# Optimization experiments

Measured on AMD Instinct MI355X. Metric: run time of the kernel, lower is better.

Reference implementation:

```python
import jax, jax.numpy as jnp
import numpy as np

BATCH, SEQ = 256, 100
DM = 256           # d_m
DI = 512           # Mamba d_inner = 2*d_m
DID = 512          # decoder d_inner = 2*d_d
N = 16             # d_state
DTR = 16           # dt_rank = ceil(d_m/16)
DCONV = 4
NLAYERS = 3


def silu(v):
    return v * jax.nn.sigmoid(v)


def setup_inputs() -> dict:
    key = jax.random.key(0)
    ks = jax.random.split(key, 20)
    rn = lambda k, s, sc=0.02: jax.random.normal(k, s, jnp.float32) * sc
    A_log = jnp.log(jnp.arange(1, N + 1, dtype=jnp.float32))  # (N,)
    return {
        'x': jax.random.normal(ks[0], (BATCH, SEQ, 8), jnp.float32),
        'W_embed': rn(ks[1], (8, DM)), 'b_embed': jnp.zeros((DM,), jnp.float32),
        'm_in_w': rn(ks[2], (DM, 2 * DI)),
        'm_conv_w': rn(ks[3], (DI, DCONV), 0.1), 'm_conv_b': jnp.zeros((DI,), jnp.float32),
        'm_xproj_w': rn(ks[4], (DI, DTR + 2 * N)),
        'm_dtproj_w': rn(ks[5], (DTR, DI), DTR ** -0.5),
        'm_dtproj_b': rn(ks[6], (DI,), 0.5) - 4.0,
        'm_A_log': jnp.broadcast_to(A_log, (DI, N)).copy(),
        'm_D': jnp.ones((DI,), jnp.float32),
        'm_out_w': rn(ks[7], (DI, DM)),
        'dec_in_w': rn(ks[8], (NLAYERS, 4, 2 * DID)), 'dec_in_b': jnp.zeros((NLAYERS, 2 * DID), jnp.float32),
        'dec_flow_w': rn(ks[9], (NLAYERS, DM, DTR + 2 * N)),
        'dec_dt_w': rn(ks[10], (NLAYERS, DTR, DID), DTR ** -0.5),
        'dec_dt_b': rn(ks[11], (NLAYERS, DID), 0.5) - 4.0,
        'dec_A_log': jnp.broadcast_to(A_log, (NLAYERS, DID, N)).copy(),
        'dec_D': jnp.ones((NLAYERS, DID), jnp.float32),
        'dec_out_w': rn(ks[12], (NLAYERS, DID, 4)), 'dec_out_b': jnp.zeros((NLAYERS, 4), jnp.float32),
    }


def _forward(x, W_embed, b_embed, m_in_w, m_conv_w, m_conv_b, m_xproj_w,
             m_dtproj_w, m_dtproj_b, m_A_log, m_D, m_out_w,
             dec_in_w, dec_in_b, dec_flow_w, dec_dt_w, dec_dt_b,
             dec_A_log, dec_D, dec_out_w, dec_out_b):
    b, l, _ = x.shape
    # ---- MambaEncoder ----
    emb = x @ W_embed + b_embed                       # (b, l, dm)
    xz = emb @ m_in_w                                 # (b, l, 2*di)
    xs, z = jnp.split(xz, 2, axis=-1)
    # causal depthwise conv1d, kernel=DCONV
    xp = jnp.pad(xs, ((0, 0), (DCONV - 1, 0), (0, 0)))
    xc = sum(xp[:, k:k + l, :] * m_conv_w[:, k] for k in range(DCONV)) + m_conv_b
    xc = silu(xc)
    proj = xc @ m_xproj_w                             # (b, l, dtr+2n)
    dt = jax.nn.softplus(proj[..., :DTR] @ m_dtproj_w + m_dtproj_b)  # (b, l, di)
    Bm = proj[..., DTR:DTR + N]                       # (b, l, n)
    Cm = proj[..., DTR + N:]
    A = -jnp.exp(m_A_log)                             # (di, n)

    def enc_step(h, inp):
        dt_t, B_t, C_t, x_t = inp                     # (b,di),(b,n),(b,n),(b,di)
        h = h * jnp.exp(dt_t[:, :, None] * A) + (dt_t * x_t)[:, :, None] * B_t[:, None, :]
        y = jnp.einsum('bdn,bn->bd', h, C_t) + m_D * x_t
        return h, y

    h0 = jnp.zeros((b, DI, N), xc.dtype)
    _, ys = jax.lax.scan(enc_step, h0,
                         (dt.transpose(1, 0, 2), Bm.transpose(1, 0, 2),
                          Cm.transpose(1, 0, 2), xc.transpose(1, 0, 2)))
    y = ys.transpose(1, 0, 2) * silu(z)               # (b, l, di)
    enc = y @ m_out_w                                 # (b, l, dm)
    flow = enc[:, -1]                                 # (b, dm) -- last token (no cls_token)

    # ---- FlowDecoder stack ----
    cur_bbox = x[:, -1, :4]
    hidden = jnp.zeros((b, DID, N), x.dtype)

    def dec_step(carry, p):
        bbox, h = carry
        in_w, in_b, flow_w, dt_w, dt_b, A_log, Dp, out_w, out_b = p
        bh = bbox @ in_w + in_b                       # (b, 2*did)
        e, r = jnp.split(bh, 2, axis=-1)
        e = silu(e)
        pf = flow @ flow_w                            # (b, dtr+2n)
        dtd = jax.nn.softplus(pf[:, :DTR] @ dt_w + dt_b)  # (b, did)
        Bp, Cp = pf[:, DTR:DTR + N], pf[:, DTR + N:]
        Ad = -jnp.exp(A_log)                          # (did, n)
        h = h * jnp.exp(dtd[:, :, None] * Ad) + e[:, :, None] * (dtd[:, :, None] * Bp[:, None, :])
        yd = jnp.einsum('bdn,bn->bd', h, Cp) + Dp * e
        yd = yd * silu(r)
        out = yd @ out_w + out_b                      # (b, 4)
        # torch code detaches cur_bbox and hidden_state between layers
        return (jax.lax.stop_gradient(out), jax.lax.stop_gradient(h)), out

    _, outs = jax.lax.scan(dec_step, (cur_bbox, hidden),
                           (dec_in_w, dec_in_b, dec_flow_w, dec_dt_w, dec_dt_b,
                            dec_A_log, dec_D, dec_out_w, dec_out_b))
    return outs[-1]                                   # final predicted bbox (b, 4)


def reference(x, W_embed, b_embed, m_in_w, m_conv_w, m_conv_b, m_xproj_w,
              m_dtproj_w, m_dtproj_b, m_A_log, m_D, m_out_w,
              dec_in_w, dec_in_b, dec_flow_w, dec_dt_w, dec_dt_b,
              dec_A_log, dec_D, dec_out_w, dec_out_b):
    return _forward(x, W_embed, b_embed, m_in_w, m_conv_w, m_conv_b, m_xproj_w,
                    m_dtproj_w, m_dtproj_b, m_A_log, m_D, m_out_w,
                    dec_in_w, dec_in_b, dec_flow_w, dec_dt_w, dec_dt_b,
                    dec_A_log, dec_D, dec_out_w, dec_out_b)
```

## Files before the change

### kernel.cpp

```cpp
#include <hip/hip_runtime.h>
#include <math.h>

#define BATCH 256
#define SEQ 100
#define DMODEL 256
#define DI 512
#define DID 512
#define NST 16
#define DTRANK 16
#define DCONV 4
#define NLAYERS 3

#define W2_OFF 0
#define B2_OFF 8192
#define WT_OFF 9216
#define CWT_OFF 33792
#define FLAG_OFF 35840
#define PROJ_OFF 35848
#define SILUZ_OFF 1264648
#define Y_OFF 1395720

__device__ __forceinline__ float silu_f(float x) { return x / (1.0f + __expf(-x)); }

#define DPP_ADD(v, ctrl, rmask) \
    v += __int_as_float(__builtin_amdgcn_update_dpp(0, __float_as_int(v), ctrl, rmask, 0xF, false))

__device__ __forceinline__ float wave64_sum(float v) {
    DPP_ADD(v, 0xB1, 0xF);
    DPP_ADD(v, 0x4E, 0xF);
    DPP_ADD(v, 0x141, 0xF);
    DPP_ADD(v, 0x140, 0xF);
    DPP_ADD(v, 0x142, 0xA);
    DPP_ADD(v, 0x143, 0xC);
    return v;
}

typedef float sf16 __attribute__((ext_vector_type(16)));
typedef float sf8 __attribute__((ext_vector_type(8)));

__device__ __forceinline__ int rfl(int v) { return __builtin_amdgcn_readfirstlane(v); }

#define SL2(dA, dB, base, offA, offB)                    \
    asm volatile("s_load_dwordx16 %0, %2, %3\n\t"        \
                 "s_load_dwordx16 %1, %2, %4"            \
                 : "=&s"(dA), "=&s"(dB)                  \
                 : "s"(base), "s"(offA), "s"(offB))
#define SLX(dX, base, off) \
    asm volatile("s_load_dwordx8 %0, %1, %2" : "=&s"(dX) : "s"(base), "s"(off))
#define SLC(dC, base, off) \
    asm volatile("s_load_dwordx16 %0, %1, %2" : "=&s"(dC) : "s"(base), "s"(off))
#define SL_WAIT()                                          \
    do {                                                   \
        asm volatile("s_waitcnt lgkmcnt(0)" ::: "memory"); \
        __builtin_amdgcn_sched_barrier(0);                 \
    } while (0)

__global__ void k_prep(const float* __restrict__ W_embed, const float* __restrict__ b_embed,
                       const float* __restrict__ m_in_w, const float* __restrict__ xproj_w,
                       const float* __restrict__ conv_w, const float* __restrict__ A_log,
                       const float* __restrict__ dec_A_log, float* __restrict__ ws,
                       int* __restrict__ flags) {
    int bid = blockIdx.x, tid = threadIdx.x;
    if (bid < 4) {
        int j = bid * 256 + tid;
        float acc[8] = {0, 0, 0, 0, 0, 0, 0, 0};
        float accb = 0.f;
        for (int c = 0; c < DMODEL; ++c) {
            float w = m_in_w[c * 1024 + j];
            accb += b_embed[c] * w;
#pragma unroll
            for (int i = 0; i < 8; ++i) acc[i] += W_embed[i * DMODEL + c] * w;
        }
#pragma unroll
        for (int i = 0; i < 8; ++i) ws[W2_OFF + i * 1024 + j] = acc[i];
        ws[B2_OFF + j] = accb;
    } else if (bid < 100) {
        int idx = (bid - 4) * 256 + tid;
        int j = idx / 512, c = idx % 512;
        ws[WT_OFF + j * 512 + c] = xproj_w[c * 48 + j];
    } else if (bid < 108) {
        int idx = (bid - 100) * 256 + tid;
        int tap = idx / 512, c = idx % 512;
        ws[CWT_OFF + tap * 512 + c] = conv_w[c * 4 + tap];
    } else {
        __shared__ int oks[2];
        if (tid == 0) { oks[0] = 1; oks[1] = 1; }
        __syncthreads();
        int bad_e = 0, bad_d = 0;
        for (int i = tid; i < DI * NST; i += 256) {
            int dd = i / NST, n = i % NST;
            float a0 = __expf(A_log[dd * NST]);
            float an = __expf(A_log[dd * NST + n]);
            if (fabsf(an - (n + 1) * a0) > 1e-4f * (n + 1)) bad_e = 1;
        }
        for (int i = tid; i < NLAYERS * DID * NST; i += 256) {
            int dd = i / NST, n = i % NST;
            float a0 = __expf(dec_A_log[dd * NST]);
            float an = __expf(dec_A_log[dd * NST + n]);
            if (fabsf(an - (n + 1) * a0) > 1e-4f * (n + 1)) bad_d = 1;
        }
        if (bad_e) atomicAnd(&oks[0], 0);
        if (bad_d) atomicAnd(&oks[1], 0);
        __syncthreads();
        if (tid == 0) { flags[0] = oks[0]; flags[1] = oks[1]; }
    }
}

__global__ void __launch_bounds__(256, 3) k_convproj(
    const float* __restrict__ x, const float* __restrict__ ws, const float* __restrict__ conv_b,
    float* __restrict__ proj_g, float* __restrict__ silu_z) {
    __shared__ __align__(16) float xs_s[23 * 512];
    __shared__ __align__(16) float proj_s[20 * 48];
    const float* W2 = ws + W2_OFF;
    const float* b2 = ws + B2_OFF;
    const float* wT = ws + WT_OFF;
    const float* cwT = ws + CWT_OFF;
    const int b = blockIdx.x / 5, tb = blockIdx.x % 5, t0 = tb * 20;
    const int tid = threadIdx.x, lane = tid & 63, wv = tid >> 6;

    {
        int c0 = tid * 2;
        float wa[8], wb[8];
#pragma unroll
        for (int i = 0; i < 8; ++i) {
            float2 wp = *(const float2*)&W2[i * 1024 + c0];
            wa[i] = wp.x;
            wb[i] = wp.y;
        }
        float2 bp = *(const float2*)&b2[c0];
        for (int r = 0; r < 23; ++r) {
            int t = t0 - 3 + r;
            float va = 0.f, vb = 0.f;
            if (t >= 0) {
                const float4* xr = (const float4*)(x + (size_t)(b * SEQ + t) * 8);
                float4 xlo = xr[0], xhi = xr[1];
                va = bp.x + xlo.x * wa[0] + xlo.y * wa[1] + xlo.z * wa[2] + xlo.w * wa[3] +
                     xhi.x * wa[4] + xhi.y * wa[5] + xhi.z * wa[6] + xhi.w * wa[7];
                vb = bp.y + xlo.x * wb[0] + xlo.y * wb[1] + xlo.z * wb[2] + xlo.w * wb[3] +
                     xhi.x * wb[4] + xhi.y * wb[5] + xhi.z * wb[6] + xhi.w * wb[7];
            }
            *(float2*)&xs_s[r * 512 + c0] = make_float2(va, vb);
        }
        if (tb == 4) {
            const float4* xr = (const float4*)(x + (size_t)(b * SEQ + SEQ - 1) * 8);
            float4 xlo = xr[0], xhi = xr[1];
            float za = b2[512 + c0], zb = b2[512 + c0 + 1];
#pragma unroll
            for (int i = 0; i < 8; ++i) {
                float xi = (i < 4) ? ((const float*)&xlo)[i] : ((const float*)&xhi)[i - 4];
                float2 wp = *(const float2*)&W2[i * 1024 + 512 + c0];
                za += xi * wp.x;
                zb += xi * wp.y;
            }
            silu_z[b * DI + c0] = silu_f(za);
            silu_z[b * DI + c0 + 1] = silu_f(zb);
        }
    }
    __syncthreads();
    const int cA = lane * 4, cB = 256 + lane * 4;
    float xcv[5][8];
    {
        float4 cwA[4], cwB[4];
#pragma unroll
        for (int tap = 0; tap < 4; ++tap) {
            cwA[tap] = *(const float4*)&cwT[tap * 512 + cA];
            cwB[tap] = *(const float4*)&cwT[tap * 512 + cB];
        }
        float4 cbA = *(const float4*)&conv_b[cA];
        float4 cbB = *(const float4*)&conv_b[cB];
#pragma unroll
        for (int q = 0; q < 5; ++q) {
            int rb = wv * 5 + q;
            float4 aA = cbA, aB = cbB;
#pragma unroll
            for (int tap = 0; tap < 4; ++tap) {
                float4 xA = *(const float4*)&xs_s[(rb + tap) * 512 + cA];
                float4 xB = *(const float4*)&xs_s[(rb + tap) * 512 + cB];
                aA.x += cwA[tap].x * xA.x; aA.y += cwA[tap].y * xA.y;
                aA.z += cwA[tap].z * xA.z; aA.w += cwA[tap].w * xA.w;
                aB.x += cwB[tap].x * xB.x; aB.y += cwB[tap].y * xB.y;
                aB.z += cwB[tap].z * xB.z; aB.w += cwB[tap].w * xB.w;
            }
            xcv[q][0] = silu_f(aA.x); xcv[q][1] = silu_f(aA.y);
            xcv[q][2] = silu_f(aA.z); xcv[q][3] = silu_f(aA.w);
            xcv[q][4] = silu_f(aB.x); xcv[q][5] = silu_f(aB.y);
            xcv[q][6] = silu_f(aB.z); xcv[q][7] = silu_f(aB.w);
        }
    }
    {
#pragma unroll 2
        for (int j = 0; j < 48; ++j) {
            float4 wA = *(const float4*)&wT[j * 512 + cA];
            float4 wB = *(const float4*)&wT[j * 512 + cB];
            float a0 = 0.f, a1 = 0.f, a2 = 0.f, a3 = 0.f, a4 = 0.f;
#pragma unroll
            for (int k = 0; k < 4; ++k) {
                float wk = ((const float*)&wA)[k];
                float wk2 = ((const float*)&wB)[k];
                a0 += xcv[0][k] * wk + xcv[0][4 + k] * wk2;
                a1 += xcv[1][k] * wk + xcv[1][4 + k] * wk2;
                a2 += xcv[2][k] * wk + xcv[2][4 + k] * wk2;
                a3 += xcv[3][k] * wk + xcv[3][4 + k] * wk2;
                a4 += xcv[4][k] * wk + xcv[4][4 + k] * wk2;
            }
            a0 = wave64_sum(a0); a1 = wave64_sum(a1); a2 = wave64_sum(a2);
            a3 = wave64_sum(a3); a4 = wave64_sum(a4);
            if (lane == 63) {
                proj_s[(wv * 5 + 0) * 48 + j] = a0;
                proj_s[(wv * 5 + 1) * 48 + j] = a1;
                proj_s[(wv * 5 + 2) * 48 + j] = a2;
                proj_s[(wv * 5 + 3) * 48 + j] = a3;
                proj_s[(wv * 5 + 4) * 48 + j] = a4;
            }
        }
    }
    __syncthreads();
    if (tid < 240) {
        float4* dst = (float4*)(proj_g + (size_t)(b * SEQ + t0) * 48);
        dst[tid] = ((const float4*)proj_s)[tid];
    }
}

#define SCAN_STEP(SA, SB, SX)                                                        \
    do {                                                                             \
        float xsv = biasc;                                                           \
        xsv = fmaf((SX)[0], w2c[0], xsv); xsv = fmaf((SX)[1], w2c[1], xsv);          \
        xsv = fmaf((SX)[2], w2c[2], xsv); xsv = fmaf((SX)[3], w2c[3], xsv);          \
        xsv = fmaf((SX)[4], w2c[4], xsv); xsv = fmaf((SX)[5], w2c[5], xsv);          \
        xsv = fmaf((SX)[6], w2c[6], xsv); xsv = fmaf((SX)[7], w2c[7], xsv);          \
        float cv = cb + win0 * cw0 + win1 * cw1 + win2 * cw2 + xsv * cw3;            \
        win0 = win1; win1 = win2; win2 = xsv;                                        \
        xcv = silu_f(cv);                                                            \
        float acc = bdt;                                                             \
        acc = fmaf((SA)[0], wr[0], acc);  acc = fmaf((SA)[1], wr[1], acc);           \
        acc = fmaf((SA)[2], wr[2], acc);  acc = fmaf((SA)[3], wr[3], acc);           \
        acc = fmaf((SA)[4], wr[4], acc);  acc = fmaf((SA)[5], wr[5], acc);           \
        acc = fmaf((SA)[6], wr[6], acc);  acc = fmaf((SA)[7], wr[7], acc);           \
        acc = fmaf((SA)[8], wr[8], acc);  acc = fmaf((SA)[9], wr[9], acc);           \
        acc = fmaf((SA)[10], wr[10], acc); acc = fmaf((SA)[11], wr[11], acc);        \
        acc = fmaf((SA)[12], wr[12], acc); acc = fmaf((SA)[13], wr[13], acc);        \
        acc = fmaf((SA)[14], wr[14], acc); acc = fmaf((SA)[15], wr[15], acc);        \
        float dtv = (acc > 20.f) ? acc : __logf(1.f + __expf(acc));                  \
        S += dtv;                                                                    \
        float sv = dtv * xcv;                                                        \
        if (fast) {                                                                  \
            float E1 = __expf(dtv * An0);                                            \
            float E2 = E1 * E1, E3 = E2 * E1, E4 = E2 * E2;                          \
            float E5 = E4 * E1, E6 = E4 * E2, E7 = E4 * E3, E8 = E4 * E4;            \
            float E9 = E8 * E1, E10 = E8 * E2, E11 = E8 * E3, E12 = E8 * E4;         \
            float E13 = E8 * E5, E14 = E8 * E6, E15 = E8 * E7, E16 = E8 * E8;        \
            h[0] = fmaf(h[0], E1, sv * (SB)[0]);   h[1] = fmaf(h[1], E2, sv * (SB)[1]); \
            h[2] = fmaf(h[2], E3, sv * (SB)[2]);   h[3] = fmaf(h[3], E4, sv * (SB)[3]); \
            h[4] = fmaf(h[4], E5, sv * (SB)[4]);   h[5] = fmaf(h[5], E6, sv * (SB)[5]); \
            h[6] = fmaf(h[6], E7, sv * (SB)[6]);   h[7] = fmaf(h[7], E8, sv * (SB)[7]); \
            h[8] = fmaf(h[8], E9, sv * (SB)[8]);   h[9] = fmaf(h[9], E10, sv * (SB)[9]); \
            h[10] = fmaf(h[10], E11, sv * (SB)[10]); h[11] = fmaf(h[11], E12, sv * (SB)[11]); \
            h[12] = fmaf(h[12], E13, sv * (SB)[12]); h[13] = fmaf(h[13], E14, sv * (SB)[13]); \
            h[14] = fmaf(h[14], E15, sv * (SB)[14]); h[15] = fmaf(h[15], E16, sv * (SB)[15]); \
        } else {                                                                     \
            _Pragma("unroll")                                                        \
            for (int n = 0; n < NST; ++n) {                                          \
                float Ann = -__expf(A_log[d * NST + n]);                             \
                h[n] = fmaf(h[n], __expf(dtv * Ann), sv * (SB)[n]);                  \
            }                                                                        \
        }                                                                            \
    } while (0)

__global__ void __launch_bounds__(512, 4) k_scan(
    const float* __restrict__ x, const float* __restrict__ ws, const float* __restrict__ conv_b,
    const float* __restrict__ proj_g, const float* __restrict__ A_log,
    const float* __restrict__ dtw, const float* __restrict__ dtb,
    const float* __restrict__ Dvec, const float* __restrict__ silu_z,
    const int* __restrict__ flags, float* __restrict__ y_g) {
    __shared__ float h1_s[256 * 17];
    const int b = blockIdx.x >> 1, dgrp = blockIdx.x & 1;
    const int tid = threadIdx.x, half = tid >> 8, dl = tid & 255;
    const int d = dgrp * 256 + dl;
    const float* W2 = ws + W2_OFF;
    const float* b2 = ws + B2_OFF;
    const float* cwT = ws + CWT_OFF;
    const float* proj_b = proj_g + (size_t)b * SEQ * 48;
    const float* x_b = x + (size_t)b * SEQ * 8;

    float w2c[8];
#pragma unroll
    for (int i = 0; i < 8; ++i) w2c[i] = W2[i * 1024 + d];
    float biasc = b2[d];
    float cw0 = cwT[d], cw1 = cwT[512 + d], cw2 = cwT[1024 + d], cw3 = cwT[1536 + d];
    float cb = conv_b[d];
    float wr[DTRANK];
#pragma unroll
    for (int r = 0; r < DTRANK; ++r) wr[r] = dtw[r * DI + d];
    float bdt = dtb[d];
    float An0 = -__expf(A_log[d * NST]);
    const bool fast = flags[0] != 0;
    float h[NST];
#pragma unroll
    for (int n = 0; n < NST; ++n) h[n] = 0.f;
    float S = 0.f, xcv = 0.f;
    const int tstart = half * 50;

    float win0 = 0.f, win1 = 0.f, win2 = 0.f;
    for (int tt = tstart - 3; tt < tstart; ++tt) {
        float v = 0.f;
        if (tt >= 0) {
            const float4* xr = (const float4*)(x_b + tt * 8);
            float4 xa = xr[0], xb4 = xr[1];
            v = biasc + xa.x * w2c[0] + xa.y * w2c[1] + xa.z * w2c[2] + xa.w * w2c[3] +
                xb4.x * w2c[4] + xb4.y * w2c[5] + xb4.z * w2c[6] + xb4.w * w2c[7];
        }
        win0 = win1; win1 = win2; win2 = v;
    }

    int poff = rfl(tstart * 192);
    int xoff = rfl(tstart * 32);
    sf16 a0, a1, b0, b1;
    sf8 ax, bx;
    SL2(a0, a1, proj_b, poff, poff + 64);
    SLX(ax, x_b, xoff);
    SL_WAIT();
    for (int it = 0; it < 25; ++it) {
        int p1 = poff + 192, x1 = xoff + 32;
        SL2(b0, b1, proj_b, p1, p1 + 64);
        SLX(bx, x_b, x1);
        SCAN_STEP(a0, a1, ax);
        SL_WAIT();
        int p2 = (it < 24) ? poff + 384 : p1;
        int x2 = (it < 24) ? xoff + 64 : x1;
        SL2(a0, a1, proj_b, p2, p2 + 64);
        SLX(ax, x_b, x2);
        SCAN_STEP(b0, b1, bx);
        SL_WAIT();
        poff += 384;
        xoff += 64;
    }

    if (half == 0) {
#pragma unroll
        for (int n = 0; n < NST; ++n) h1_s[dl * 17 + n] = h[n];
    }
    __syncthreads();
    if (half == 1) {
        sf16 cC;
        SLC(cC, proj_b, (SEQ - 1) * 192 + 128);
        SL_WAIT();
        float yv = Dvec[d] * xcv;
        if (fast) {
            float G1 = __expf(S * An0);
            float G2 = G1 * G1, G3 = G2 * G1, G4 = G2 * G2;
            float G5 = G4 * G1, G6 = G4 * G2, G7 = G4 * G3, G8 = G4 * G4;
            float G9 = G8 * G1, G10 = G8 * G2, G11 = G8 * G3, G12 = G8 * G4;
            float G13 = G8 * G5, G14 = G8 * G6, G15 = G8 * G7, G16 = G8 * G8;
            float Gs[NST] = {G1, G2, G3, G4, G5, G6, G7, G8,
                             G9, G10, G11, G12, G13, G14, G15, G16};
#pragma unroll
            for (int n = 0; n < NST; ++n) {
                float hf = fmaf(h1_s[dl * 17 + n], Gs[n], h[n]);
                yv = fmaf(hf, cC[n], yv);
            }
        } else {
#pragma unroll
            for (int n = 0; n < NST; ++n) {
                float Ann = -__expf(A_log[d * NST + n]);
                float hf = fmaf(h1_s[dl * 17 + n], __expf(S * Ann), h[n]);
                yv = fmaf(hf, cC[n], yv);
            }
        }
        y_g[(size_t)b * DI + d] = yv * silu_z[(size_t)b * DI + d];
    }
}

__global__ void __launch_bounds__(512, 2) k_flowdec(
    const float* __restrict__ x, const float* __restrict__ y_g,
    const float* __restrict__ m_out_w, const float* __restrict__ dec_in_w,
    const float* __restrict__ dec_in_b, const float* __restrict__ dec_flow_w,
    const float* __restrict__ dec_dt_w, const float* __restrict__ dec_dt_b,
    const float* __restrict__ dec_A_log, const float* __restrict__ dec_D,
    const float* __restrict__ dec_out_w, const float* __restrict__ dec_out_b,
    const int* __restrict__ flags, float* __restrict__ out) {
    __shared__ __align__(16) float y_s[DI];
    __shared__ __align__(16) float pf_s[48];
    __shared__ float red_s[DMODEL];
    __shared__ float flow_s[DMODEL];
    __shared__ float bbox_s[4];
    __shared__ float dred_s[8][4];
    const int b = blockIdx.x, tid = threadIdx.x, d = tid;
    const int lane = tid & 63, wv = tid >> 6;
    const bool dfast = flags[1] != 0;
    y_s[d] = y_g[(size_t)b * DI + d];
    if (tid < 4) bbox_s[tid] = x[(size_t)(b * SEQ + SEQ - 1) * 8 + tid];
    __syncthreads();
    {
        int j = tid >> 1, p = tid & 1;
        float fa = 0.f;
#pragma unroll 4
        for (int i = 0; i < 64; ++i) {
            int c = p * 256 + 4 * i;
            float4 yq = *(const float4*)&y_s[c];
            fa += yq.x * m_out_w[(c + 0) * DMODEL + j];
            fa += yq.y * m_out_w[(c + 1) * DMODEL + j];
            fa += yq.z * m_out_w[(c + 2) * DMODEL + j];
            fa += yq.w * m_out_w[(c + 3) * DMODEL + j];
        }
        if (p == 1) red_s[j] = fa;
        __syncthreads();
        if (p == 0) flow_s[j] = fa + red_s[j];
    }
    float h[NST];
#pragma unroll
    for (int n = 0; n < NST; ++n) h[n] = 0.f;
    __syncthreads();
    for (int L = 0; L < NLAYERS; ++L) {
        float epre = dec_in_b[L * 1024 + d];
        float rpre = dec_in_b[L * 1024 + 512 + d];
#pragma unroll
        for (int i = 0; i < 4; ++i) {
            float bx = bbox_s[i];
            epre += bx * dec_in_w[(L * 4 + i) * 1024 + d];
            rpre += bx * dec_in_w[(L * 4 + i) * 1024 + 512 + d];
        }
        float e = silu_f(epre);
        float fl4[4];
#pragma unroll
        for (int k = 0; k < 4; ++k) fl4[k] = flow_s[lane + 64 * k];
        float pj[6];
#pragma unroll
        for (int jj = 0; jj < 6; ++jj) {
            float a = 0.f;
#pragma unroll
            for (int k = 0; k < 4; ++k)
                a += fl4[k] * dec_flow_w[L * DMODEL * 48 + (lane + 64 * k) * 48 + wv * 6 + jj];
            pj[jj] = wave64_sum(a);
        }
        if (lane == 63) {
#pragma unroll
            for (int jj = 0; jj < 6; ++jj) pf_s[wv * 6 + jj] = pj[jj];
        }
        __syncthreads();
        float4 p0 = *(const float4*)&pf_s[0];
        float4 p1 = *(const float4*)&pf_s[4];
        float4 p2 = *(const float4*)&pf_s[8];
        float4 p3 = *(const float4*)&pf_s[12];
        float dtd = dec_dt_b[L * DID + d];
        dtd += p0.x * dec_dt_w[(L * 16 + 0) * DID + d] + p0.y * dec_dt_w[(L * 16 + 1) * DID + d] +
               p0.z * dec_dt_w[(L * 16 + 2) * DID + d] + p0.w * dec_dt_w[(L * 16 + 3) * DID + d];
        dtd += p1.x * dec_dt_w[(L * 16 + 4) * DID + d] + p1.y * dec_dt_w[(L * 16 + 5) * DID + d] +
               p1.z * dec_dt_w[(L * 16 + 6) * DID + d] + p1.w * dec_dt_w[(L * 16 + 7) * DID + d];
        dtd += p2.x * dec_dt_w[(L * 16 + 8) * DID + d] + p2.y * dec_dt_w[(L * 16 + 9) * DID + d] +
               p2.z * dec_dt_w[(L * 16 + 10) * DID + d] + p2.w * dec_dt_w[(L * 16 + 11) * DID + d];
        dtd += p3.x * dec_dt_w[(L * 16 + 12) * DID + d] + p3.y * dec_dt_w[(L * 16 + 13) * DID + d] +
               p3.z * dec_dt_w[(L * 16 + 14) * DID + d] + p3.w * dec_dt_w[(L * 16 + 15) * DID + d];
        dtd = (dtd > 20.f) ? dtd : __logf(1.f + __expf(dtd));
        float4 B0 = *(const float4*)&pf_s[16];
        float4 B1 = *(const float4*)&pf_s[20];
        float4 B2 = *(const float4*)&pf_s[24];
        float4 B3 = *(const float4*)&pf_s[28];
        float4 C0 = *(const float4*)&pf_s[32];
        float4 C1 = *(const float4*)&pf_s[36];
        float4 C2 = *(const float4*)&pf_s[40];
        float4 C3 = *(const float4*)&pf_s[44];
        float Bv[NST] = {B0.x, B0.y, B0.z, B0.w, B1.x, B1.y, B1.z, B1.w,
                         B2.x, B2.y, B2.z, B2.w, B3.x, B3.y, B3.z, B3.w};
        float Cv[NST] = {C0.x, C0.y, C0.z, C0.w, C1.x, C1.y, C1.z, C1.w,
                         C2.x, C2.y, C2.z, C2.w, C3.x, C3.y, C3.z, C3.w};
        float yd = 0.f;
        if (dfast) {
            float Ad0 = -__expf(dec_A_log[(L * DID + d) * NST]);
            float E1 = __expf(dtd * Ad0);
            float E2 = E1 * E1, E3 = E2 * E1, E4 = E2 * E2;
            float E5 = E4 * E1, E6 = E4 * E2, E7 = E4 * E3, E8 = E4 * E4;
            float E9 = E8 * E1, E10 = E8 * E2, E11 = E8 * E3, E12 = E8 * E4;
            float E13 = E8 * E5, E14 = E8 * E6, E15 = E8 * E7, E16 = E8 * E8;
            float Es[NST] = {E1, E2, E3, E4, E5, E6, E7, E8,
                             E9, E10, E11, E12, E13, E14, E15, E16};
#pragma unroll
            for (int n = 0; n < NST; ++n) {
                h[n] = fmaf(h[n], Es[n], e * (dtd * Bv[n]));
                yd += h[n] * Cv[n];
            }
        } else {
#pragma unroll
            for (int n = 0; n < NST; ++n) {
                float Adn = -__expf(dec_A_log[(L * DID + d) * NST + n]);
                h[n] = fmaf(h[n], __expf(dtd * Adn), e * (dtd * Bv[n]));
                yd += h[n] * Cv[n];
            }
        }
        yd += dec_D[L * DID + d] * e;
        yd *= silu_f(rpre);
#pragma unroll
        for (int jo = 0; jo < 4; ++jo) {
            float v = wave64_sum(yd * dec_out_w[(L * DID + d) * 4 + jo]);
            if (lane == 63) dred_s[wv][jo] = v;
        }
        __syncthreads();
        if (tid < 4) {
            float a2 = dec_out_b[L * 4 + tid];
#pragma unroll
            for (int w = 0; w < 8; ++w) a2 += dred_s[w][tid];
            bbox_s[tid] = a2;
            if (L == NLAYERS - 1) out[b * 4 + tid] = a2;
        }
        __syncthreads();
    }
}

extern "C" void kernel_launch(void* const* d_in, const int* in_sizes, int n_in,
                              void* d_out, int out_size, void* d_ws, size_t ws_size,
                              hipStream_t stream) {
    const float* x          = (const float*)d_in[0];
    const float* W_embed    = (const float*)d_in[1];
    const float* b_embed    = (const float*)d_in[2];
    const float* m_in_w     = (const float*)d_in[3];
    const float* m_conv_w   = (const float*)d_in[4];
    const float* m_conv_b   = (const float*)d_in[5];
    const float* m_xproj_w  = (const float*)d_in[6];
    const float* m_dtproj_w = (const float*)d_in[7];
    const float* m_dtproj_b = (const float*)d_in[8];
    const float* m_A_log    = (const float*)d_in[9];
    const float* m_D        = (const float*)d_in[10];
    const float* m_out_w    = (const float*)d_in[11];
    const float* dec_in_w   = (const float*)d_in[12];
    const float* dec_in_b   = (const float*)d_in[13];
    const float* dec_flow_w = (const float*)d_in[14];
    const float* dec_dt_w   = (const float*)d_in[15];
    const float* dec_dt_b   = (const float*)d_in[16];
    const float* dec_A_log  = (const float*)d_in[17];
    const float* dec_D      = (const float*)d_in[18];
    const float* dec_out_w  = (const float*)d_in[19];
    const float* dec_out_b  = (const float*)d_in[20];

    float* ws = (float*)d_ws;
    int* flags = (int*)(ws + FLAG_OFF);
    float* proj_g = ws + PROJ_OFF;
    float* siluz = ws + SILUZ_OFF;
    float* y_g = ws + Y_OFF;

    k_prep<<<109, 256, 0, stream>>>(W_embed, b_embed, m_in_w, m_xproj_w, m_conv_w,
                                    m_A_log, dec_A_log, ws, flags);
    k_convproj<<<BATCH * 5, 256, 0, stream>>>(x, ws, m_conv_b, proj_g, siluz);
    k_scan<<<BATCH * 2, 512, 0, stream>>>(x, ws, m_conv_b, proj_g, m_A_log, m_dtproj_w,
                                          m_dtproj_b, m_D, siluz, flags, y_g);
    k_flowdec<<<BATCH, 512, 0, stream>>>(x, y_g, m_out_w, dec_in_w, dec_in_b, dec_flow_w,
                                         dec_dt_w, dec_dt_b, dec_A_log, dec_D, dec_out_w,
                                         dec_out_b, flags, (float*)d_out);
}
```

Measured before the change: 148.5 us.

## Restructure conv+xproj kernel to per-timestep accumulation and transpose out_proj weights

The conv+x-projection kernel is rewritten so each block covers half a sequence (50 timesteps). Channels are processed in 128-wide LDS tiles, and each lane owns one timestep and accumulates 6 projection outputs from a regrouped weight layout. This replaces the per-projection wave-wide DPP reductions with lane-local FMA accumulation, at the cost of redundant weight loads across lanes and more barriers. Separately, m_out_w is pre-transposed in the prep kernel so the flow projection in the decoder reads contiguous float4 rows.

Measured after the change: 201.2 us. 35.5% more time.

```diff
diff --git a/kernel.cpp b/kernel.cpp
--- a/kernel.cpp
+++ b/kernel.cpp
@@ -13,12 +13,13 @@
 
 #define W2_OFF 0
 #define B2_OFF 8192
-#define WT_OFF 9216
+#define WTJ_OFF 9216
 #define CWT_OFF 33792
 #define FLAG_OFF 35840
 #define PROJ_OFF 35848
 #define SILUZ_OFF 1264648
 #define Y_OFF 1395720
+#define MOWT_OFF 1526792
 
 __device__ __forceinline__ float silu_f(float x) { return x / (1.0f + __expf(-x)); }
 
@@ -58,8 +59,8 @@
 __global__ void k_prep(const float* __restrict__ W_embed, const float* __restrict__ b_embed,
                        const float* __restrict__ m_in_w, const float* __restrict__ xproj_w,
                        const float* __restrict__ conv_w, const float* __restrict__ A_log,
-                       const float* __restrict__ dec_A_log, float* __restrict__ ws,
-                       int* __restrict__ flags) {
+                       const float* __restrict__ dec_A_log, const float* __restrict__ m_out_w,
+                       float* __restrict__ ws, int* __restrict__ flags) {
     int bid = blockIdx.x, tid = threadIdx.x;
     if (bid < 4) {
         int j = bid * 256 + tid;
@@ -75,14 +76,14 @@
         for (int i = 0; i < 8; ++i) ws[W2_OFF + i * 1024 + j] = acc[i];
         ws[B2_OFF + j] = accb;
     } else if (bid < 100) {
-        int idx = (bid - 4) * 256 + tid;
-        int j = idx / 512, c = idx % 512;
-        ws[WT_OFF + j * 512 + c] = xproj_w[c * 48 + j];
+        int o = (bid - 4) * 256 + tid;
+        int jg = o / 3072, r = o % 3072, c = r / 6, jj = r % 6;
+        ws[WTJ_OFF + o] = xproj_w[c * 48 + jg * 6 + jj];
     } else if (bid < 108) {
         int idx = (bid - 100) * 256 + tid;
         int tap = idx / 512, c = idx % 512;
         ws[CWT_OFF + tap * 512 + c] = conv_w[c * 4 + tap];
-    } else {
+    } else if (bid == 108) {
         __shared__ int oks[2];
         if (tid == 0) { oks[0] = 1; oks[1] = 1; }
         __syncthreads();
@@ -103,121 +104,103 @@
         if (bad_d) atomicAnd(&oks[1], 0);
         __syncthreads();
         if (tid == 0) { flags[0] = oks[0]; flags[1] = oks[1]; }
+    } else {
+        int idx = (bid - 109) * 256 + tid;
+        int c = idx >> 8, j = idx & 255;
+        ws[MOWT_OFF + j * 512 + c] = m_out_w[idx];
     }
 }
 
-__global__ void __launch_bounds__(256, 3) k_convproj(
+#define XST 132
+__global__ void __launch_bounds__(512, 4) k_convproj(
     const float* __restrict__ x, const float* __restrict__ ws, const float* __restrict__ conv_b,
-    float* __restrict__ proj_g, float* __restrict__ silu_z) {
-    __shared__ __align__(16) float xs_s[23 * 512];
-    __shared__ __align__(16) float proj_s[20 * 48];
-    const float* W2 = ws + W2_OFF;
-    const float* b2 = ws + B2_OFF;
-    const float* wT = ws + WT_OFF;
+    const float* __restrict__ W2g, float* __restrict__ proj_g, float* __restrict__ silu_z) {
+    __shared__ float W2_l[8 * 512];
+    __shared__ float b2_l[512];
+    __shared__ float x_l[53 * 8];
+    __shared__ __align__(16) float xcb[53 * XST];
     const float* cwT = ws + CWT_OFF;
-    const int b = blockIdx.x / 5, tb = blockIdx.x % 5, t0 = tb * 20;
+    const float* wtj = ws + WTJ_OFF;
+    const int b = blockIdx.x >> 1, half = blockIdx.x & 1;
     const int tid = threadIdx.x, lane = tid & 63, wv = tid >> 6;
-
-    {
-        int c0 = tid * 2;
-        float wa[8], wb[8];
-#pragma unroll
-        for (int i = 0; i < 8; ++i) {
-            float2 wp = *(const float2*)&W2[i * 1024 + c0];
-            wa[i] = wp.x;
-            wb[i] = wp.y;
-        }
-        float2 bp = *(const float2*)&b2[c0];
-        for (int r = 0; r < 23; ++r) {
-            int t = t0 - 3 + r;
-            float va = 0.f, vb = 0.f;
+    const float* x_b = x + (size_t)b * SEQ * 8;
+
+    for (int i = tid; i < 4096; i += 512) {
+        int r = i >> 9, c = i & 511;
+        W2_l[i] = W2g[r * 1024 + c];
+    }
+    b2_l[tid] = ws[B2_OFF + tid];
+    if (tid < 424) {
+        int r = tid >> 3, k = tid & 7;
+        int t = half * 50 + r - 3;
+        x_l[tid] = (t >= 0) ? x_b[t * 8 + k] : 0.f;
+    }
+    __syncthreads();
+
+    if (half == 1) {
+        float z = ws[B2_OFF + 512 + tid];
+#pragma unroll
+        for (int i = 0; i < 8; ++i) z += x_l[52 * 8 + i] * W2g[i * 1024 + 512 + tid];
+        silu_z[b * DI + tid] = silu_f(z);
+    }
+
+    const int jg = wv;
+    float acc[6] = {0.f, 0.f, 0.f, 0.f, 0.f, 0.f};
+    const int tl = (lane < 50) ? lane : 49;
+
+    for (int ct = 0; ct < 4; ++ct) {
+        __syncthreads();
+        for (int i = tid; i < 53 * 128; i += 512) {
+            int r = i >> 7, cc = i & 127, cg = ct * 128 + cc;
+            int t = half * 50 + r - 3;
+            float v = 0.f;
             if (t >= 0) {
-                const float4* xr = (const float4*)(x + (size_t)(b * SEQ + t) * 8);
-                float4 xlo = xr[0], xhi = xr[1];
-                va = bp.x + xlo.x * wa[0] + xlo.y * wa[1] + xlo.z * wa[2] + xlo.w * wa[3] +
-                     xhi.x * wa[4] + xhi.y * wa[5] + xhi.z * wa[6] + xhi.w * wa[7];
-                vb = bp.y + xlo.x * wb[0] + xlo.y * wb[1] + xlo.z * wb[2] + xlo.w * wb[3] +
-                     xhi.x * wb[4] + xhi.y * wb[5] + xhi.z * wb[6] + xhi.w * wb[7];
+                v = b2_l[cg];
+#pragma unroll
+                for (int k = 0; k < 8; ++k) v = fmaf(x_l[r * 8 + k], W2_l[k * 512 + cg], v);
             }
-            *(float2*)&xs_s[r * 512 + c0] = make_float2(va, vb);
-        }
-        if (tb == 4) {
-            const float4* xr = (const float4*)(x + (size_t)(b * SEQ + SEQ - 1) * 8);
-            float4 xlo = xr[0], xhi = xr[1];
-            float za = b2[512 + c0], zb = b2[512 + c0 + 1];
-#pragma unroll
-            for (int i = 0; i < 8; ++i) {
-                float xi = (i < 4) ? ((const float*)&xlo)[i] : ((const float*)&xhi)[i - 4];
-                float2 wp = *(const float2*)&W2[i * 1024 + 512 + c0];
-                za += xi * wp.x;
-                zb += xi * wp.y;
+            xcb[r * XST + cc] = v;
+        }
+        __syncthreads();
+        float cv[13];
+#pragma unroll
+        for (int k = 0; k < 13; ++k) {
+            int i = tid + k * 512;
+            int ii = (i < 6400) ? i : 6399;
+            int r = ii >> 7, cc = ii & 127, cg = ct * 128 + cc;
+            float a = conv_b[cg];
+#pragma unroll
+            for (int tap = 0; tap < 4; ++tap)
+                a = fmaf(cwT[tap * 512 + cg], xcb[(r + tap) * XST + cc], a);
+            cv[k] = silu_f(a);
+        }
+        __syncthreads();
+#pragma unroll
+        for (int k = 0; k < 13; ++k) {
+            int i = tid + k * 512;
+            if (i < 6400) xcb[((i >> 7) + 3) * XST + (i & 127)] = cv[k];
+        }
+        __syncthreads();
+        const float* wbase = wtj + jg * 3072 + ct * 768;
+        const float* xrow = &xcb[(tl + 3) * XST];
+#pragma unroll 2
+        for (int qq = 0; qq < 32; ++qq) {
+            float4 xv = *(const float4*)&xrow[qq * 4];
+            const float* wq = wbase + qq * 24;
+#pragma unroll
+            for (int cc = 0; cc < 4; ++cc) {
+                float xc1 = (cc == 0) ? xv.x : (cc == 1) ? xv.y : (cc == 2) ? xv.z : xv.w;
+#pragma unroll
+                for (int jj = 0; jj < 6; ++jj)
+                    acc[jj] = fmaf(wq[cc * 6 + jj], xc1, acc[jj]);
             }
-            silu_z[b * DI + c0] = silu_f(za);
-            silu_z[b * DI + c0 + 1] = silu_f(zb);
-        }
-    }
-    __syncthreads();
-    const int cA = lane * 4, cB = 256 + lane * 4;
-    float xcv[5][8];
-    {
-        float4 cwA[4], cwB[4];
-#pragma unroll
-        for (int tap = 0; tap < 4; ++tap) {
-            cwA[tap] = *(const float4*)&cwT[tap * 512 + cA];
-            cwB[tap] = *(const float4*)&cwT[tap * 512 + cB];
-        }
-        float4 cbA = *(const float4*)&conv_b[cA];
-        float4 cbB = *(const float4*)&conv_b[cB];
-#pragma unroll
-        for (int q = 0; q < 5; ++q) {
-            int rb = wv * 5 + q;
-            float4 aA = cbA, aB = cbB;
-#pragma unroll
-            for (int tap = 0; tap < 4; ++tap) {
-                float4 xA = *(const float4*)&xs_s[(rb + tap) * 512 + cA];
-                float4 xB = *(const float4*)&xs_s[(rb + tap) * 512 + cB];
-                aA.x += cwA[tap].x * xA.x; aA.y += cwA[tap].y * xA.y;
-                aA.z += cwA[tap].z * xA.z; aA.w += cwA[tap].w * xA.w;
-                aB.x += cwB[tap].x * xB.x; aB.y += cwB[tap].y * xB.y;
-                aB.z += cwB[tap].z * xB.z; aB.w += cwB[tap].w * xB.w;
-            }
-            xcv[q][0] = silu_f(aA.x); xcv[q][1] = silu_f(aA.y);
-            xcv[q][2] = silu_f(aA.z); xcv[q][3] = silu_f(aA.w);
-            xcv[q][4] = silu_f(aB.x); xcv[q][5] = silu_f(aB.y);
-            xcv[q][6] = silu_f(aB.z); xcv[q][7] = silu_f(aB.w);
-        }
-    }
-    {
-#pragma unroll 2
-        for (int j = 0; j < 48; ++j) {
-            float4 wA = *(const float4*)&wT[j * 512 + cA];
-            float4 wB = *(const float4*)&wT[j * 512 + cB];
-            float a0 = 0.f, a1 = 0.f, a2 = 0.f, a3 = 0.f, a4 = 0.f;
-#pragma unroll
-            for (int k = 0; k < 4; ++k) {
-                float wk = ((const float*)&wA)[k];
-                float wk2 = ((const float*)&wB)[k];
-                a0 += xcv[0][k] * wk + xcv[0][4 + k] * wk2;
-                a1 += xcv[1][k] * wk + xcv[1][4 + k] * wk2;
-                a2 += xcv[2][k] * wk + xcv[2][4 + k] * wk2;
-                a3 += xcv[3][k] * wk + xcv[3][4 + k] * wk2;
-                a4 += xcv[4][k] * wk + xcv[4][4 + k] * wk2;
-            }
-            a0 = wave64_sum(a0); a1 = wave64_sum(a1); a2 = wave64_sum(a2);
-            a3 = wave64_sum(a3); a4 = wave64_sum(a4);
-            if (lane == 63) {
-                proj_s[(wv * 5 + 0) * 48 + j] = a0;
-                proj_s[(wv * 5 + 1) * 48 + j] = a1;
-                proj_s[(wv * 5 + 2) * 48 + j] = a2;
-                proj_s[(wv * 5 + 3) * 48 + j] = a3;
-                proj_s[(wv * 5 + 4) * 48 + j] = a4;
-            }
-        }
-    }
-    __syncthreads();
-    if (tid < 240) {
-        float4* dst = (float4*)(proj_g + (size_t)(b * SEQ + t0) * 48);
-        dst[tid] = ((const float4*)proj_s)[tid];
+        }
+    }
+    if (lane < 50) {
+        float* dst = proj_g + ((size_t)b * SEQ + half * 50 + lane) * 48 + jg * 6;
+        *(float2*)(dst + 0) = make_float2(acc[0], acc[1]);
+        *(float2*)(dst + 2) = make_float2(acc[2], acc[3]);
+        *(float2*)(dst + 4) = make_float2(acc[4], acc[5]);
     }
 }
 
@@ -372,7 +355,7 @@
 
 __global__ void __launch_bounds__(512, 2) k_flowdec(
     const float* __restrict__ x, const float* __restrict__ y_g,
-    const float* __restrict__ m_out_w, const float* __restrict__ dec_in_w,
+    const float* __restrict__ mowt, const float* __restrict__ dec_in_w,
     const float* __restrict__ dec_in_b, const float* __restrict__ dec_flow_w,
     const float* __restrict__ dec_dt_w, const float* __restrict__ dec_dt_b,
     const float* __restrict__ dec_A_log, const float* __restrict__ dec_D,
@@ -392,15 +375,14 @@
     __syncthreads();
     {
         int j = tid >> 1, p = tid & 1;
+        const float* wrow = mowt + (size_t)j * 512 + p * 256;
+        const float* yrow = &y_s[p * 256];
         float fa = 0.f;
 #pragma unroll 4
         for (int i = 0; i < 64; ++i) {
-            int c = p * 256 + 4 * i;
-            float4 yq = *(const float4*)&y_s[c];
-            fa += yq.x * m_out_w[(c + 0) * DMODEL + j];
-            fa += yq.y * m_out_w[(c + 1) * DMODEL + j];
-            fa += yq.z * m_out_w[(c + 2) * DMODEL + j];
-            fa += yq.w * m_out_w[(c + 3) * DMODEL + j];
+            float4 wq = *(const float4*)&wrow[4 * i];
+            float4 yq = *(const float4*)&yrow[4 * i];
+            fa += wq.x * yq.x + wq.y * yq.y + wq.z * yq.z + wq.w * yq.w;
         }
         if (p == 1) red_s[j] = fa;
         __syncthreads();
@@ -535,13 +517,14 @@
     float* proj_g = ws + PROJ_OFF;
     float* siluz = ws + SILUZ_OFF;
     float* y_g = ws + Y_OFF;
-
-    k_prep<<<109, 256, 0, stream>>>(W_embed, b_embed, m_in_w, m_xproj_w, m_conv_w,
-                                    m_A_log, dec_A_log, ws, flags);
-    k_convproj<<<BATCH * 5, 256, 0, stream>>>(x, ws, m_conv_b, proj_g, siluz);
+    float* mowt = ws + MOWT_OFF;
+
+    k_prep<<<621, 256, 0, stream>>>(W_embed, b_embed, m_in_w, m_xproj_w, m_conv_w,
+                                    m_A_log, dec_A_log, m_out_w, ws, flags);
+    k_convproj<<<BATCH * 2, 512, 0, stream>>>(x, ws, m_conv_b, ws + W2_OFF, proj_g, siluz);
     k_scan<<<BATCH * 2, 512, 0, stream>>>(x, ws, m_conv_b, proj_g, m_A_log, m_dtproj_w,
                                           m_dtproj_b, m_D, siluz, flags, y_g);
-    k_flowdec<<<BATCH, 512, 0, stream>>>(x, y_g, m_out_w, dec_in_w, dec_in_b, dec_flow_w,
+    k_flowdec<<<BATCH, 512, 0, stream>>>(x, y_g, mowt, dec_in_w, dec_in_b, dec_flow_w,
                                          dec_dt_w, dec_dt_b, dec_A_log, dec_D, dec_out_w,
                                          dec_out_b, flags, (float*)d_out);
 }
```
